# Optimization experiments

Measured on AMD Instinct MI355X. Metric: run time of the kernel, lower is better.

## Reference

```python
import jax, jax.numpy as jnp
import numpy as np

N, G = 10000, 200          # nodes, graphs
EL, EG = 160000, 500000    # local / global edges
S, V = 256, 64             # scalar / vector hidden dims
NA, NB = 16, 5             # atom types, bond types


def _lin(k, i, o):
    return (jax.random.normal(k, (i, o), jnp.float32) / np.sqrt(i))


def scatter_mean(vals, idx, num_segments):
    # vals: [N, ...]; idx: [N] int
    sums = jax.ops.segment_sum(vals, idx, num_segments=num_segments)
    cnt = jax.ops.segment_sum(jnp.ones((vals.shape[0],), vals.dtype), idx,
                              num_segments=num_segments)
    cnt = jnp.maximum(cnt, 1.0).reshape((-1,) + (1,) * (vals.ndim - 1))
    return sums / cnt


def calc_edge_attrs(edge_index, pos):
    src, tgt = edge_index[0], edge_index[1]
    r = pos[tgt] - pos[src]                      # [E,3]
    a = (pos[tgt] * pos[src]).sum(-1)            # [E]
    d = jnp.sqrt(jnp.clip((r ** 2).sum(-1), 1e-6))
    r_norm = r / d[:, None]
    return d, a, r_norm


def setup_inputs() -> dict:
    key = jax.random.key(0)
    ks = jax.random.split(key, 24)
    inp = {}
    inp["x"] = jax.random.normal(ks[0], (N, NA), jnp.float32)
    inp["t"] = jax.random.uniform(ks[1], (G, 1), jnp.float32)
    inp["pos"] = jax.random.normal(ks[2], (N, 3), jnp.float32)
    eil = jax.random.randint(ks[3], (2, EL), 0, N)
    eig = jax.random.randint(ks[4], (2, EG), 0, N)
    # avoid self-edges so edge distances are strictly positive (safe sqrt grads)
    eig = eig.at[1].set(jnp.where(eig[1] == eig[0], (eig[1] + 1) % N, eig[1]))
    eil = eil.at[1].set(jnp.where(eil[1] == eil[0], (eil[1] + 1) % N, eil[1]))
    inp["edge_index_local"] = eil
    inp["edge_index_global"] = eig
    inp["edge_attr_global"] = jax.random.normal(ks[5], (EG, NB), jnp.float32)
    inp["batch"] = jnp.sort(jax.random.randint(ks[6], (N,), 0, G))
    # learned parameters
    inp["W_time"], inp["b_time"] = _lin(ks[7], 1, S), jnp.zeros((S,), jnp.float32)
    inp["W_atom"], inp["b_atom"] = _lin(ks[8], NA, S), jnp.zeros((S,), jnp.float32)
    inp["W_at"], inp["b_at"] = _lin(ks[9], S, S), jnp.zeros((S,), jnp.float32)
    inp["W_shared"], inp["b_shared"] = _lin(ks[10], S, S), jnp.zeros((S,), jnp.float32)
    inp["W_b0"], inp["b_b0"] = _lin(ks[11], S + 1, S), jnp.zeros((S,), jnp.float32)
    inp["W_b1"], inp["b_b1"] = _lin(ks[12], S, 2 * NB), jnp.zeros((2 * NB,), jnp.float32)
    inp["W_coord"] = _lin(ks[13], V, 2)           # no bias
    inp["W_atoms"], inp["b_atoms"] = _lin(ks[14], S, 2 * NA), jnp.zeros((2 * NA,), jnp.float32)
    return inp


def reference(x, t, pos, edge_attr_global, W_time, b_time, W_atom, b_atom,
              W_at, b_at, W_shared, b_shared, W_b0, b_b0, W_b1, b_b1,
              W_coord, W_atoms, b_atoms,
              edge_index_local, edge_index_global, batch):
    # --- trunk: center positions, embed atoms + time ---
    pos = pos - scatter_mean(pos, batch, G)[batch]
    temb = t @ W_time + b_time                    # [G,S]
    tnode = temb[batch]                           # [N,S]
    s = x @ W_atom + b_atom
    s = (s + tnode) @ W_at + b_at                 # [N,S]
    # --- edge attrs (gather-compute pattern feeding the GNN) ---
    d_l, a_l, rn_l = calc_edge_attrs(edge_index_local, pos)
    d_g, a_g, rn_g = calc_edge_attrs(edge_index_global, pos)
    # GNN stand-in (identity on s, v, p): v initialized to zeros as in original
    v = jnp.zeros((N, 3, V), s.dtype)
    # --- prediction head ---
    s = jax.nn.silu(s @ W_shared + b_shared)
    j, i = edge_index_global[0], edge_index_global[1]
    d = jnp.sqrt(((pos[i] - pos[j]) ** 2).sum(-1, keepdims=True))  # [EG,1]
    edge = jnp.concatenate([s[i] + s[j], d], axis=-1)              # [EG,S+1]
    bonds = jax.nn.silu(edge @ W_b0 + b_b0) @ W_b1 + b_b1          # [EG,2*NB]
    bonds_pred, bonds_eps = bonds[:, :NB], bonds[:, NB:]
    coords = jnp.einsum('nkv,vo->nko', v, W_coord)                 # [N,3,2]
    coords = coords - scatter_mean(coords, batch, G)[batch]
    coords_eps0, coords_eps1 = coords[..., 0], coords[..., 1]      # [N,3]
    atoms = s @ W_atoms + b_atoms                                  # [N,2*NA]
    atoms_eps, atoms_pred = atoms[:, :NA], atoms[:, NA:]
    pos_c = pos - scatter_mean(pos, batch, G)[batch]
    coords_pred = pos_c + coords_eps1
    return (coords_pred, coords_eps0, atoms_pred, atoms_eps,
            bonds_pred, bonds_eps, d_l, rn_l, a_g, rn_g)
```

## Files before the change

### kernel.cpp

```cpp
#include <hip/hip_runtime.h>
#include <hip/hip_bf16.h>

typedef __hip_bfloat16 bf16;
typedef short bf16x8 __attribute__((ext_vector_type(8)));
typedef float f32x4 __attribute__((ext_vector_type(4)));
typedef float f32x2 __attribute__((ext_vector_type(2)));
typedef _Float16 f16x2 __attribute__((ext_vector_type(2)));
typedef _Float16 f16x8 __attribute__((ext_vector_type(8)));
typedef __fp16 fp16x2 __attribute__((ext_vector_type(2)));

#define N_NODES  10000
#define G_GRAPHS 200
#define EL_EDGES 160000
#define EG_EDGES 500000
#define S_DIM    256
#define APAD     264

#define BONDS2        7813
#define LOCAL_BLOCKS  625

#define WS_FLAG   0
#define WS_POSC   1024
#define WS_WD     31232
#define WS_W1F    31488
#define WS_BB0R   33536
#define WS_BB1    34304
#define WS_WATOM  34560
#define WS_WTIME  38656
#define WS_BTIME  38912
#define WS_BATOM  39168
#define WS_BAT    39424
#define WS_BSH    39680
#define WS_BATOMS 39936
#define WS_T      40000
#define WS_X      40448
#define WT_AT     200448
#define WT_SH     233216
#define WT_B0     265984
#define WT_ATOMS  298752
#define WS_H      303968
#define WS_END_FLOATS 944224

#define CHAN(S)    ((((S) >> 6) << 6) + (((S) & 3) << 4) + (((S) & 63) >> 2))

#define O_CPRED 0
#define O_CEPS  30000
#define O_APRED 60000
#define O_AEPS  220000
#define O_BPRED 380000
#define O_BEPS  2880000
#define O_DL    5380000
#define O_RNL   5540000
#define O_AG    6020000
#define O_RNG   6520000

__device__ __forceinline__ float b2f(bf16 v) { return __bfloat162float(v); }
__device__ __forceinline__ bf16  f2b(float v) { return __float2bfloat16(v); }
__device__ __forceinline__ unsigned short bbits(float v) {
    bf16 b = f2b(v);
    return *reinterpret_cast<unsigned short*>(&b);
}
__device__ __forceinline__ unsigned short h16bits(float v) {
    _Float16 h = (_Float16)v;
    return *reinterpret_cast<unsigned short*>(&h);
}
__device__ __forceinline__ float ldin(const void* p, int idx, int isf32) {
    return isf32 ? ((const float*)p)[idx] : b2f(((const bf16*)p)[idx]);
}
__device__ __forceinline__ void stout(void* out, int f32o, size_t idx, float v) {
    if (f32o) ((float*)out)[idx] = v;
    else      ((bf16*)out)[idx]  = f2b(v);
}
__device__ __forceinline__ float silu(float p) {
    return p * __builtin_amdgcn_rcpf(1.0f + __expf(-p));
}
__device__ __forceinline__ f32x2 silu2(f32x2 p) {
    f32x2 u;
    u[0] = p[0] * __builtin_amdgcn_rcpf(1.0f + __expf(-p[0]));
    u[1] = p[1] * __builtin_amdgcn_rcpf(1.0f + __expf(-p[1]));
    return u;
}
__device__ __forceinline__ int dtype_f32(const void* tt) {
    const unsigned short* q = (const unsigned short*)tt;
    int c = 0;
#pragma unroll
    for (int z = 0; z < 32; ++z) c += (q[z] >= 0x4000) ? 1 : 0;
    return c > 0;
}

__global__ void k_prep(const void* __restrict__ x, const void* __restrict__ tt,
                       const void* __restrict__ W_time, const void* __restrict__ b_time,
                       const void* __restrict__ W_atom, const void* __restrict__ b_atom,
                       const void* __restrict__ W_at, const void* __restrict__ b_at,
                       const void* __restrict__ W_shared, const void* __restrict__ b_shared,
                       const void* __restrict__ W_b0, const void* __restrict__ b_b0,
                       const void* __restrict__ W_b1, const void* __restrict__ b_b1,
                       const void* __restrict__ W_atoms, const void* __restrict__ b_atoms,
                       float* __restrict__ ws) {
    const int t = blockIdx.x * blockDim.x + threadIdx.x;
    const int f = dtype_f32(tt);
    if (t == 0) ws[WS_FLAG] = f ? 1.0f : 0.0f;
    if (t < 65536) {
        const int k = t >> 8, n = t & 255;
        ((unsigned short*)(ws + WT_AT))[n * 256 + k] = bbits(ldin(W_at, t, f));
        ((unsigned short*)(ws + WT_SH))[n * 256 + k] = bbits(ldin(W_shared, t, f));
        ((unsigned short*)(ws + WT_B0))[n * 256 + k] = bbits(ldin(W_b0, t, f));
    }
    if (t < 160000) ws[WS_X + t] = ldin(x, t, f);
    if (t < 8192) {
        const int k = t >> 5, n = t & 31;
        ((unsigned short*)(ws + WT_ATOMS))[n * 256 + k] = bbits(ldin(W_atoms, t, f));
    }
    if (t < 4096) {
        const int i = t & 7, lc = (t >> 3) & 15, q = (t >> 7) & 3, ts = t >> 9;
        const int s = ts * 32 + q * 8 + i;
        float v = (lc < 10) ? ldin(W_b1, CHAN(s) * 10 + lc, f) : 0.0f;
        ((unsigned short*)(ws + WS_W1F))[t] = h16bits(v);
    }
    if (t < 4096) ws[WS_WATOM + t] = ldin(W_atom, t, f);
    if (t < 256) {
        ws[WS_WD + t]   = ldin(W_b0, 65536 + CHAN(t), f);
        ws[WS_BB0R + t] = ldin(b_b0, t, f);
        ws[WS_WTIME + t] = ldin(W_time, t, f);
        ws[WS_BTIME + t] = ldin(b_time, t, f);
        ws[WS_BATOM + t] = ldin(b_atom, t, f);
        ws[WS_BAT + t]   = ldin(b_at, t, f);
        ws[WS_BSH + t]   = ldin(b_shared, t, f);
    }
    if (t < 200) ws[WS_T + t] = ldin(tt, t, f);
    if (t < 32)  ws[WS_BATOMS + t] = ldin(b_atoms, t, f);
    if (t < 16)  ws[WS_BB1 + t] = (t < 10) ? ldin(b_b1, t, f) : 0.0f;
}

__global__ void k_pos(const void* __restrict__ pos, const int* __restrict__ batch,
                      float* __restrict__ ws, void* __restrict__ out) {
    const int g = blockIdx.x;
    const int f32o = ws[WS_FLAG] != 0.0f;
    __shared__ int s_lo, s_hi;
    __shared__ float wsum[4][3];
    __shared__ float mean[3];
    if (threadIdx.x == 0) {
        int lo = 0, hi = N_NODES;
        while (lo < hi) { int m = (lo + hi) >> 1; if (batch[m] < g) lo = m + 1; else hi = m; }
        s_lo = lo;
        int lo2 = lo; hi = N_NODES;
        while (lo2 < hi) { int m = (lo2 + hi) >> 1; if (batch[m] < g + 1) lo2 = m + 1; else hi = m; }
        s_hi = lo2;
    }
    __syncthreads();
    const int lo = s_lo, hi = s_hi, cnt = hi - lo;
    float sx = 0.f, sy = 0.f, sz = 0.f;
    for (int n = lo + threadIdx.x; n < hi; n += 256) {
        sx += ldin(pos, n * 3 + 0, f32o);
        sy += ldin(pos, n * 3 + 1, f32o);
        sz += ldin(pos, n * 3 + 2, f32o);
    }
#pragma unroll
    for (int off = 32; off > 0; off >>= 1) {
        sx += __shfl_down(sx, off);
        sy += __shfl_down(sy, off);
        sz += __shfl_down(sz, off);
    }
    if ((threadIdx.x & 63) == 0) {
        wsum[threadIdx.x >> 6][0] = sx;
        wsum[threadIdx.x >> 6][1] = sy;
        wsum[threadIdx.x >> 6][2] = sz;
    }
    __syncthreads();
    if (threadIdx.x == 0) {
        float inv = 1.0f / (float)max(cnt, 1);
        mean[0] = (wsum[0][0] + wsum[1][0] + wsum[2][0] + wsum[3][0]) * inv;
        mean[1] = (wsum[0][1] + wsum[1][1] + wsum[2][1] + wsum[3][1]) * inv;
        mean[2] = (wsum[0][2] + wsum[1][2] + wsum[2][2] + wsum[3][2]) * inv;
    }
    __syncthreads();
    for (int n = lo + threadIdx.x; n < hi; n += 256) {
#pragma unroll
        for (int k = 0; k < 3; ++k) {
            float p = ldin(pos, n * 3 + k, f32o) - mean[k];
            ws[WS_POSC + n * 3 + k] = p;
            stout(out, f32o, O_CPRED + n * 3 + k, p);
            stout(out, f32o, O_CEPS + n * 3 + k, 0.0f);
        }
    }
}

__global__ __launch_bounds__(256) void k_node(
    const int* __restrict__ batch, const float* __restrict__ ws,
    unsigned int* __restrict__ h_out, void* __restrict__ out) {
    __shared__ unsigned short actA[16][APAD];
    __shared__ unsigned short actB[16][APAD];
    const int tid = threadIdx.x;
    const int wave = tid >> 6, lane = tid & 63;
    const int quad = lane >> 4, l16 = lane & 15;
    const int row0 = blockIdx.x * 16;

    {
        const int r = tid >> 4;
        const int c0 = (tid & 15) * 16;
        const int g = row0 + r;
        float tb = ws[WS_T + batch[g]];
        float xr[16];
#pragma unroll
        for (int k = 0; k < 16; ++k) xr[k] = ws[WS_X + g * 16 + k];
        for (int cc = 0; cc < 16; cc += 4) {
            const int c = c0 + cc;
            float a0 = ws[WS_BATOM + c + 0] + tb * ws[WS_WTIME + c + 0] + ws[WS_BTIME + c + 0];
            float a1 = ws[WS_BATOM + c + 1] + tb * ws[WS_WTIME + c + 1] + ws[WS_BTIME + c + 1];
            float a2 = ws[WS_BATOM + c + 2] + tb * ws[WS_WTIME + c + 2] + ws[WS_BTIME + c + 2];
            float a3 = ws[WS_BATOM + c + 3] + tb * ws[WS_WTIME + c + 3] + ws[WS_BTIME + c + 3];
#pragma unroll
            for (int k = 0; k < 16; ++k) {
                float4 w4 = *(const float4*)(ws + WS_WATOM + k * S_DIM + c);
                a0 += xr[k] * w4.x; a1 += xr[k] * w4.y;
                a2 += xr[k] * w4.z; a3 += xr[k] * w4.w;
            }
            actA[r][c + 0] = bbits(a0); actA[r][c + 1] = bbits(a1);
            actA[r][c + 2] = bbits(a2); actA[r][c + 3] = bbits(a3);
        }
    }
    __syncthreads();

    const unsigned short* wt_at = (const unsigned short*)(ws + WT_AT);
    const unsigned short* wt_sh = (const unsigned short*)(ws + WT_SH);
    const unsigned short* wt_b0 = (const unsigned short*)(ws + WT_B0);
    const unsigned short* wt_am = (const unsigned short*)(ws + WT_ATOMS);
    const int n0 = wave * 64;

    {
        f32x4 acc[4] = {};
        for (int kk = 0; kk < S_DIM; kk += 32) {
            const int k = kk + quad * 8;
            bf16x8 a = *(const bf16x8*)&actA[l16][k];
#pragma unroll
            for (int nt = 0; nt < 4; ++nt) {
                bf16x8 b = *(const bf16x8*)(wt_at + (size_t)(n0 + nt * 16 + l16) * S_DIM + k);
                acc[nt] = __builtin_amdgcn_mfma_f32_16x16x32_bf16(a, b, acc[nt], 0, 0, 0);
            }
        }
#pragma unroll
        for (int nt = 0; nt < 4; ++nt) {
            const int n = n0 + nt * 16 + l16;
            const float bv = ws[WS_BAT + n];
#pragma unroll
            for (int r = 0; r < 4; ++r)
                actB[quad * 4 + r][n] = bbits(acc[nt][r] + bv);
        }
    }
    __syncthreads();

    {
        f32x4 acc[4] = {};
        for (int kk = 0; kk < S_DIM; kk += 32) {
            const int k = kk + quad * 8;
            bf16x8 a = *(const bf16x8*)&actB[l16][k];
#pragma unroll
            for (int nt = 0; nt < 4; ++nt) {
                bf16x8 b = *(const bf16x8*)(wt_sh + (size_t)(n0 + nt * 16 + l16) * S_DIM + k);
                acc[nt] = __builtin_amdgcn_mfma_f32_16x16x32_bf16(a, b, acc[nt], 0, 0, 0);
            }
        }
        __syncthreads();
#pragma unroll
        for (int nt = 0; nt < 4; ++nt) {
            const int n = n0 + nt * 16 + l16;
            const float bv = ws[WS_BSH + n];
#pragma unroll
            for (int r = 0; r < 4; ++r)
                actA[quad * 4 + r][n] = bbits(silu(acc[nt][r] + bv));
        }
    }
    __syncthreads();

    {
        f32x4 acc[4] = {};
        for (int kk = 0; kk < S_DIM; kk += 32) {
            const int k = kk + quad * 8;
            bf16x8 a = *(const bf16x8*)&actA[l16][k];
#pragma unroll
            for (int nt = 0; nt < 4; ++nt) {
                bf16x8 b = *(const bf16x8*)(wt_b0 + (size_t)(n0 + nt * 16 + l16) * S_DIM + k);
                acc[nt] = __builtin_amdgcn_mfma_f32_16x16x32_bf16(a, b, acc[nt], 0, 0, 0);
            }
        }
        float bh[4];
#pragma unroll
        for (int nt = 0; nt < 4; ++nt) bh[nt] = 0.5f * ws[WS_BB0R + n0 + nt * 16 + l16];
#pragma unroll
        for (int r = 0; r < 4; ++r) {
            const int g = row0 + quad * 4 + r;
            int w = 0;
            w = __builtin_amdgcn_cvt_pk_fp8_f32(acc[0][r] + bh[0], acc[1][r] + bh[1], w, false);
            w = __builtin_amdgcn_cvt_pk_fp8_f32(acc[2][r] + bh[2], acc[3][r] + bh[3], w, true);
            h_out[(size_t)g * 64 + wave * 16 + l16] = (unsigned int)w;
        }
    }

    if (wave < 2) {
        f32x4 acc = {};
        const int n = wave * 16 + l16;
        for (int kk = 0; kk < S_DIM; kk += 32) {
            const int k = kk + quad * 8;
            bf16x8 a = *(const bf16x8*)&actA[l16][k];
            bf16x8 b = *(const bf16x8*)(wt_am + (size_t)n * S_DIM + k);
            acc = __builtin_amdgcn_mfma_f32_16x16x32_bf16(a, b, acc, 0, 0, 0);
        }
        const float bv = ws[WS_BATOMS + n];
        const int f32o = ws[WS_FLAG] != 0.0f;
#pragma unroll
        for (int r = 0; r < 4; ++r) {
            const int g = row0 + quad * 4 + r;
            float v = acc[r] + bv;
            if (n < 16) stout(out, f32o, O_AEPS + (size_t)g * 16 + n, v);
            else        stout(out, f32o, O_APRED + (size_t)g * 16 + (n - 16), v);
        }
    }
}

union U8 { f16x8 v; fp16x2 p[4]; };

__global__ __launch_bounds__(256, 4) void k_edges(const int* __restrict__ eig,
                                                  const int* __restrict__ eil,
                                                  const float* __restrict__ ws,
                                                  const unsigned char* __restrict__ h,
                                                  void* __restrict__ out) {
    const int f32o = ws[WS_FLAG] != 0.0f;

    if (blockIdx.x >= BONDS2) {
        const int e = (blockIdx.x - BONDS2) * 256 + threadIdx.x;
        const float* posc = ws + WS_POSC;
        const int s = eil[e];
        const int t = eil[EL_EDGES + e];
        float rx = posc[t * 3 + 0] - posc[s * 3 + 0];
        float ry = posc[t * 3 + 1] - posc[s * 3 + 1];
        float rz = posc[t * 3 + 2] - posc[s * 3 + 2];
        float dsq = rx * rx + ry * ry + rz * rz;
        float d = sqrtf(fmaxf(dsq, 1e-6f));
        float inv = 1.0f / d;
        stout(out, f32o, O_DL + e, d);
        stout(out, f32o, O_RNL + (size_t)e * 3 + 0, rx * inv);
        stout(out, f32o, O_RNL + (size_t)e * 3 + 1, ry * inv);
        stout(out, f32o, O_RNL + (size_t)e * 3 + 2, rz * inv);
        return;
    }

    const int wave = threadIdx.x >> 6, lane = threadIdx.x & 63;
    const int quad = lane >> 4, l16 = lane & 15;
    const int e0 = blockIdx.x * 64 + wave * 16;
    if (e0 >= EG_EDGES) return;

    const int e = e0 + l16;
    const int j = eig[e];
    const int i = eig[EG_EDGES + e];

    const float* posc = ws + WS_POSC;
    float pix = posc[i * 3 + 0], piy = posc[i * 3 + 1], piz = posc[i * 3 + 2];
    float pjx = posc[j * 3 + 0], pjy = posc[j * 3 + 1], pjz = posc[j * 3 + 2];
    float rx = pix - pjx, ry = piy - pjy, rz = piz - pjz;
    float dsq = rx * rx + ry * ry + rz * rz;
    float dgeo = sqrtf(dsq);
    if (quad == 0) {
        float ag = pix * pjx + piy * pjy + piz * pjz;
        float inv = 1.0f / sqrtf(fmaxf(dsq, 1e-6f));
        stout(out, f32o, O_AG + e, ag);
        stout(out, f32o, O_RNG + (size_t)e * 3 + 0, rx * inv);
        stout(out, f32o, O_RNG + (size_t)e * 3 + 1, ry * inv);
        stout(out, f32o, O_RNG + (size_t)e * 3 + 2, rz * inv);
    }

    const f32x2 d2 = {dgeo, dgeo};
    const unsigned char* hi_row = h + (size_t)i * 256;
    const unsigned char* hj_row = h + (size_t)j * 256;
    const _Float16* w1f = (const _Float16*)(ws + WS_W1F) + (quad * 16 + l16) * 8;

    f32x4 acc = {};
#pragma unroll 2
    for (int t = 0; t < 8; ++t) {
        const int k = quad * 8 + t * 32;
        uint2 ua = *(const uint2*)(hi_row + k);
        uint2 ub = *(const uint2*)(hj_row + k);
        float4 wA = *(const float4*)(ws + WS_WD + k);
        float4 wB = *(const float4*)(ws + WS_WD + k + 4);
        f16x8 WF = *(const f16x8*)(w1f + t * 512);
        f32x2 a01 = __builtin_amdgcn_cvt_pk_f32_fp8((int)ua.x, false);
        f32x2 a23 = __builtin_amdgcn_cvt_pk_f32_fp8((int)ua.x, true);
        f32x2 a45 = __builtin_amdgcn_cvt_pk_f32_fp8((int)ua.y, false);
        f32x2 a67 = __builtin_amdgcn_cvt_pk_f32_fp8((int)ua.y, true);
        f32x2 b01 = __builtin_amdgcn_cvt_pk_f32_fp8((int)ub.x, false);
        f32x2 b23 = __builtin_amdgcn_cvt_pk_f32_fp8((int)ub.x, true);
        f32x2 b45 = __builtin_amdgcn_cvt_pk_f32_fp8((int)ub.y, false);
        f32x2 b67 = __builtin_amdgcn_cvt_pk_f32_fp8((int)ub.y, true);
        f32x2 p01 = (a01 + b01) + d2 * (f32x2){wA.x, wA.y};
        f32x2 p23 = (a23 + b23) + d2 * (f32x2){wA.z, wA.w};
        f32x2 p45 = (a45 + b45) + d2 * (f32x2){wB.x, wB.y};
        f32x2 p67 = (a67 + b67) + d2 * (f32x2){wB.z, wB.w};
        f32x2 u01 = silu2(p01);
        f32x2 u23 = silu2(p23);
        f32x2 u45 = silu2(p45);
        f32x2 u67 = silu2(p67);
        U8 U;
        U.p[0] = __builtin_amdgcn_cvt_pkrtz(u01[0], u01[1]);
        U.p[1] = __builtin_amdgcn_cvt_pkrtz(u23[0], u23[1]);
        U.p[2] = __builtin_amdgcn_cvt_pkrtz(u45[0], u45[1]);
        U.p[3] = __builtin_amdgcn_cvt_pkrtz(u67[0], u67[1]);
        acc = __builtin_amdgcn_mfma_f32_16x16x32_f16(U.v, WF, acc, 0, 0, 0);
    }

    if (l16 < 10) {
        const float bv = ws[WS_BB1 + l16];
#pragma unroll
        for (int r = 0; r < 4; ++r) {
            const int er = e0 + quad * 4 + r;
            float v = acc[r] + bv;
            if (l16 < 5) stout(out, f32o, O_BPRED + (size_t)er * 5 + l16, v);
            else         stout(out, f32o, O_BEPS + (size_t)er * 5 + (l16 - 5), v);
        }
    }
}

extern "C" void kernel_launch(void* const* d_in, const int* in_sizes, int n_in,
                              void* d_out, int out_size, void* d_ws, size_t ws_size,
                              hipStream_t stream) {
    const void* x        = d_in[0];
    const void* t        = d_in[1];
    const void* pos      = d_in[2];
    const int*  eil      = (const int*)d_in[3];
    const int*  eig      = (const int*)d_in[4];
    const int*  batch    = (const int*)d_in[6];
    const void* W_time   = d_in[7];
    const void* b_time   = d_in[8];
    const void* W_atom   = d_in[9];
    const void* b_atom   = d_in[10];
    const void* W_at     = d_in[11];
    const void* b_at     = d_in[12];
    const void* W_shared = d_in[13];
    const void* b_shared = d_in[14];
    const void* W_b0     = d_in[15];
    const void* b_b0     = d_in[16];
    const void* W_b1     = d_in[17];
    const void* b_b1     = d_in[18];
    const void* W_atoms  = d_in[20];
    const void* b_atoms  = d_in[21];
    (void)in_sizes; (void)n_in; (void)out_size;

    const size_t NEED = (size_t)WS_END_FLOATS * sizeof(float);
    if (ws_size < NEED) return;

    float* ws = (float*)d_ws;
    unsigned int* hbuf = (unsigned int*)(ws + WS_H);

    k_prep<<<640, 256, 0, stream>>>(x, t, W_time, b_time, W_atom, b_atom,
                                    W_at, b_at, W_shared, b_shared, W_b0, b_b0,
                                    W_b1, b_b1, W_atoms, b_atoms, ws);
    k_pos<<<G_GRAPHS, 256, 0, stream>>>(pos, batch, ws, d_out);
    k_node<<<N_NODES / 16, 256, 0, stream>>>(batch, ws, hbuf, d_out);
    k_edges<<<BONDS2 + LOCAL_BLOCKS, 256, 0, stream>>>(
        eig, eil, ws, (const unsigned char*)hbuf, d_out);
}
```

Baseline: 259.6 us.

## Stage gathered node rows in swizzled LDS and compute edge SiLU in fp16

The edge kernel now gathers the two 256-byte fp8 node rows per edge into a per-wave shared-memory tile with wide, coalesced 16-byte loads and an XOR swizzle, instead of scattered 8-byte global reads per lane. The pre-activation sum, distance term and SiLU are now computed in packed fp16 using hardware exp2 and rcp instructions, and the distance weight vector is stored as fp16. This aims to cut global gather inefficiency and VALU cost. In exchange it uses 32 KB of LDS per block, which may limit occupancy, and it lowers the precision of the activation path.

```diff
diff --git a/kernel.cpp b/kernel.cpp
--- a/kernel.cpp
+++ b/kernel.cpp
@@ -21,7 +21,7 @@
 
 #define WS_FLAG   0
 #define WS_POSC   1024
-#define WS_WD     31232
+#define WS_WDH    31232
 #define WS_W1F    31488
 #define WS_BB0R   33536
 #define WS_BB1    34304
@@ -74,11 +74,34 @@
 __device__ __forceinline__ float silu(float p) {
     return p * __builtin_amdgcn_rcpf(1.0f + __expf(-p));
 }
-__device__ __forceinline__ f32x2 silu2(f32x2 p) {
-    f32x2 u;
-    u[0] = p[0] * __builtin_amdgcn_rcpf(1.0f + __expf(-p[0]));
-    u[1] = p[1] * __builtin_amdgcn_rcpf(1.0f + __expf(-p[1]));
-    return u;
+__device__ __forceinline__ _Float16 h_exp2(_Float16 x) {
+    _Float16 r;
+    asm("v_exp_f16 %0, %1" : "=v"(r) : "v"(x));
+    return r;
+}
+__device__ __forceinline__ _Float16 h_rcp(_Float16 x) {
+    _Float16 r;
+    asm("v_rcp_f16 %0, %1" : "=v"(r) : "v"(x));
+    return r;
+}
+__device__ __forceinline__ f16x2 hsilu2(f16x2 p) {
+    const _Float16 nl = (_Float16)(-1.44269504f);
+    f16x2 q = p * (f16x2){nl, nl};
+    f16x2 ex;
+    ex[0] = h_exp2(q[0]);
+    ex[1] = h_exp2(q[1]);
+    f16x2 den = ex + (f16x2){(_Float16)1.0f, (_Float16)1.0f};
+    f16x2 rc;
+    rc[0] = h_rcp(den[0]);
+    rc[1] = h_rcp(den[1]);
+    return p * rc;
+}
+template<bool HI>
+__device__ __forceinline__ f16x2 dec2(int enc) {
+    f32x2 f = __builtin_amdgcn_cvt_pk_f32_fp8(enc, HI);
+    union { fp16x2 a; f16x2 b; } u;
+    u.a = __builtin_amdgcn_cvt_pkrtz(f[0], f[1]);
+    return u.b;
 }
 __device__ __forceinline__ int dtype_f32(const void* tt) {
     const unsigned short* q = (const unsigned short*)tt;
@@ -119,7 +142,7 @@
     }
     if (t < 4096) ws[WS_WATOM + t] = ldin(W_atom, t, f);
     if (t < 256) {
-        ws[WS_WD + t]   = ldin(W_b0, 65536 + CHAN(t), f);
+        ((unsigned short*)(ws + WS_WDH))[t] = h16bits(ldin(W_b0, 65536 + CHAN(t), f));
         ws[WS_BB0R + t] = ldin(b_b0, t, f);
         ws[WS_WTIME + t] = ldin(W_time, t, f);
         ws[WS_BTIME + t] = ldin(b_time, t, f);
@@ -317,13 +340,14 @@
     }
 }
 
-union U8 { f16x8 v; fp16x2 p[4]; };
+union U8 { f16x8 v; f16x2 p[4]; };
 
 __global__ __launch_bounds__(256, 4) void k_edges(const int* __restrict__ eig,
                                                   const int* __restrict__ eil,
                                                   const float* __restrict__ ws,
                                                   const unsigned char* __restrict__ h,
                                                   void* __restrict__ out) {
+    __shared__ unsigned char sm[4][32][256];
     const int f32o = ws[WS_FLAG] != 0.0f;
 
     if (blockIdx.x >= BONDS2) {
@@ -349,10 +373,22 @@
     const int e0 = blockIdx.x * 64 + wave * 16;
     if (e0 >= EG_EDGES) return;
 
+    unsigned char* smw = &sm[wave][0][0];
+
+#pragma unroll
+    for (int p = 0; p < 8; ++p) {
+        const int r16 = (p & 3) * 4 + quad;
+        const int es = e0 + r16;
+        const int node = (p < 4) ? eig[EG_EDGES + es]
+                                 : eig[es];
+        const int row = (p < 4) ? r16 : 16 + r16;
+        uint4 v = *(const uint4*)(h + (size_t)node * 256 + l16 * 16);
+        *(uint4*)(smw + row * 256 + ((l16 ^ (r16 >> 1)) << 4)) = v;
+    }
+
     const int e = e0 + l16;
     const int j = eig[e];
     const int i = eig[EG_EDGES + e];
-
     const float* posc = ws + WS_POSC;
     float pix = posc[i * 3 + 0], piy = posc[i * 3 + 1], piz = posc[i * 3 + 2];
     float pjx = posc[j * 3 + 0], pjy = posc[j * 3 + 1], pjz = posc[j * 3 + 2];
@@ -368,41 +404,31 @@
         stout(out, f32o, O_RNG + (size_t)e * 3 + 2, rz * inv);
     }
 
-    const f32x2 d2 = {dgeo, dgeo};
-    const unsigned char* hi_row = h + (size_t)i * 256;
-    const unsigned char* hj_row = h + (size_t)j * 256;
+    const _Float16 hd = (_Float16)dgeo;
+    const f16x2 d2h = {hd, hd};
+    const unsigned short* wdh = (const unsigned short*)(ws + WS_WDH);
     const _Float16* w1f = (const _Float16*)(ws + WS_W1F) + (quad * 16 + l16) * 8;
+    const int r2 = l16 >> 1;
+    const unsigned char* rowA = smw + l16 * 256;
+    const unsigned char* rowB = smw + (16 + l16) * 256;
 
     f32x4 acc = {};
 #pragma unroll 2
     for (int t = 0; t < 8; ++t) {
-        const int k = quad * 8 + t * 32;
-        uint2 ua = *(const uint2*)(hi_row + k);
-        uint2 ub = *(const uint2*)(hj_row + k);
-        float4 wA = *(const float4*)(ws + WS_WD + k);
-        float4 wB = *(const float4*)(ws + WS_WD + k + 4);
+        const int off = (((2 * t + (quad >> 1)) ^ r2) << 4) + ((quad & 1) << 3);
+        uint2 ua = *(const uint2*)(rowA + off);
+        uint2 ub = *(const uint2*)(rowB + off);
+        U8 W;  W.v = *(const f16x8*)(wdh + t * 32 + quad * 8);
         f16x8 WF = *(const f16x8*)(w1f + t * 512);
-        f32x2 a01 = __builtin_amdgcn_cvt_pk_f32_fp8((int)ua.x, false);
-        f32x2 a23 = __builtin_amdgcn_cvt_pk_f32_fp8((int)ua.x, true);
-        f32x2 a45 = __builtin_amdgcn_cvt_pk_f32_fp8((int)ua.y, false);
-        f32x2 a67 = __builtin_amdgcn_cvt_pk_f32_fp8((int)ua.y, true);
-        f32x2 b01 = __builtin_amdgcn_cvt_pk_f32_fp8((int)ub.x, false);
-        f32x2 b23 = __builtin_amdgcn_cvt_pk_f32_fp8((int)ub.x, true);
-        f32x2 b45 = __builtin_amdgcn_cvt_pk_f32_fp8((int)ub.y, false);
-        f32x2 b67 = __builtin_amdgcn_cvt_pk_f32_fp8((int)ub.y, true);
-        f32x2 p01 = (a01 + b01) + d2 * (f32x2){wA.x, wA.y};
-        f32x2 p23 = (a23 + b23) + d2 * (f32x2){wA.z, wA.w};
-        f32x2 p45 = (a45 + b45) + d2 * (f32x2){wB.x, wB.y};
-        f32x2 p67 = (a67 + b67) + d2 * (f32x2){wB.z, wB.w};
-        f32x2 u01 = silu2(p01);
-        f32x2 u23 = silu2(p23);
-        f32x2 u45 = silu2(p45);
-        f32x2 u67 = silu2(p67);
+        f16x2 s0 = dec2<false>((int)ua.x) + dec2<false>((int)ub.x);
+        f16x2 s1 = dec2<true>((int)ua.x)  + dec2<true>((int)ub.x);
+        f16x2 s2 = dec2<false>((int)ua.y) + dec2<false>((int)ub.y);
+        f16x2 s3 = dec2<true>((int)ua.y)  + dec2<true>((int)ub.y);
         U8 U;
-        U.p[0] = __builtin_amdgcn_cvt_pkrtz(u01[0], u01[1]);
-        U.p[1] = __builtin_amdgcn_cvt_pkrtz(u23[0], u23[1]);
-        U.p[2] = __builtin_amdgcn_cvt_pkrtz(u45[0], u45[1]);
-        U.p[3] = __builtin_amdgcn_cvt_pkrtz(u67[0], u67[1]);
+        U.p[0] = hsilu2(s0 + d2h * W.p[0]);
+        U.p[1] = hsilu2(s1 + d2h * W.p[1]);
+        U.p[2] = hsilu2(s2 + d2h * W.p[2]);
+        U.p[3] = hsilu2(s3 + d2h * W.p[3]);
         acc = __builtin_amdgcn_mfma_f32_16x16x32_f16(U.v, WF, acc, 0, 0, 0);
     }
 
```

Result: faster. 229.6 us (-11.6%).
